# Kernel optimization log

Measured on AMD Instinct MI355X. Metric: run time of the kernel, lower is better.

## Reference

```python
import jax, jax.numpy as jnp
import numpy as np

B, N_OCR, N_OBJ, D, H, L, DFF = 64, 64, 192, 768, 12, 4, 2048
DH = D // H
EPS = 1e-5  # torch LayerNorm default


def _ln(x, g, b):
    m = jnp.mean(x, axis=-1, keepdims=True)
    v = jnp.mean(jnp.square(x - m), axis=-1, keepdims=True)
    return (x - m) * jax.lax.rsqrt(v + EPS) * g + b


def setup_inputs():
    key = jax.random.key(0)
    ks = iter(jax.random.split(key, 32))
    s = 0.02
    f = lambda shape: jax.random.normal(next(ks), shape, jnp.float32) * s
    return {
        "ocr_feats": jax.random.normal(next(ks), (B, N_OCR, D), jnp.float32),
        "obj_feats": jax.random.normal(next(ks), (B, N_OBJ, D), jnp.float32),
        "ocr_dvs": jax.random.uniform(next(ks), (B, N_OCR, 1), jnp.float32, 0.1, 2.0),
        "obj_dvs": jax.random.uniform(next(ks), (B, N_OBJ, 1), jnp.float32, 0.1, 2.0),
        # SemanticAttentionDeFUM projections
        "sa_wq": f((D, D)), "sa_bq": jnp.zeros((D,), jnp.float32),
        "sa_wk": f((D, D)), "sa_bk": jnp.zeros((D,), jnp.float32),
        "sa_wv": f((D, D)), "sa_bv": jnp.zeros((D,), jnp.float32),
        # outer LayerNorm
        "ln0_g": jnp.ones((D,), jnp.float32), "ln0_b": jnp.zeros((D,), jnp.float32),
        # stacked TransformerEncoder layer params (post-norm, batch_first)
        "qkv_w": f((L, 3 * D, D)), "qkv_b": jnp.zeros((L, 3 * D), jnp.float32),
        "out_w": f((L, D, D)), "out_b": jnp.zeros((L, D), jnp.float32),
        "ln1_g": jnp.ones((L, D), jnp.float32), "ln1_b": jnp.zeros((L, D), jnp.float32),
        "ff1_w": f((L, DFF, D)), "ff1_b": jnp.zeros((L, DFF), jnp.float32),
        "ff2_w": f((L, D, DFF)), "ff2_b": jnp.zeros((L, D), jnp.float32),
        "ln2_g": jnp.ones((L, D), jnp.float32), "ln2_b": jnp.zeros((L, D), jnp.float32),
    }


def reference(ocr_feats, obj_feats, ocr_dvs, obj_dvs,
              sa_wq, sa_bq, sa_wk, sa_bk, sa_wv, sa_bv,
              ln0_g, ln0_b,
              qkv_w, qkv_b, out_w, out_b, ln1_g, ln1_b,
              ff1_w, ff1_b, ff2_w, ff2_b, ln2_g, ln2_b):
    num_ocr = ocr_feats.shape[1]
    x = jnp.concatenate([ocr_feats, obj_feats], axis=1)       # B,N,D
    dv = jnp.concatenate([ocr_dvs, obj_dvs], axis=1)[..., 0]  # B,N
    # vectorized cal_relative_depth_map: log(max(dv_i,dv_j)/min(dv_i,dv_j))
    R = jnp.log(jnp.maximum(dv[:, :, None], dv[:, None, :]) /
                jnp.minimum(dv[:, :, None], dv[:, None, :]))  # B,N,N
    # semantic attention: scores A and values V
    q = jnp.einsum('bnd,ed->bne', x, sa_wq) + sa_bq
    k = jnp.einsum('bnd,ed->bne', x, sa_wk) + sa_bk
    v = jnp.einsum('bnd,ed->bne', x, sa_wv) + sa_bv
    A = jnp.einsum('bqd,bkd->bqk', q, k) / jnp.sqrt(jnp.float32(D))
    att = jax.nn.softmax(A + R, axis=-1)
    h = _ln(x + jnp.einsum('bqk,bkd->bqd', att, v), ln0_g, ln0_b)

    def layer(h, p):
        qw, qb, ow, ob, l1g, l1b, f1w, f1b, f2w, f2b, l2g, l2b = p
        Bn, N, _ = h.shape
        qkv = jnp.einsum('bnd,ed->bne', h, qw) + qb            # B,N,3D
        qh, kh, vh = jnp.split(qkv, 3, axis=-1)
        qh = qh.reshape(Bn, N, H, DH).transpose(0, 2, 1, 3)
        kh = kh.reshape(Bn, N, H, DH).transpose(0, 2, 1, 3)
        vh = vh.reshape(Bn, N, H, DH).transpose(0, 2, 1, 3)
        sc = jnp.einsum('bhqd,bhkd->bhqk', qh, kh) / jnp.sqrt(jnp.float32(DH))
        o = jnp.einsum('bhqk,bhkd->bhqd', jax.nn.softmax(sc, axis=-1), vh)
        o = o.transpose(0, 2, 1, 3).reshape(Bn, N, D)
        o = jnp.einsum('bnd,ed->bne', o, ow) + ob
        h = _ln(h + o, l1g, l1b)
        ff = jnp.einsum('bnd,fd->bnf', h, f1w) + f1b
        ff = jax.nn.gelu(ff, approximate=False)  # torch 'gelu' = exact erf gelu
        ff = jnp.einsum('bnf,df->bnd', ff, f2w) + f2b
        h = _ln(h + ff, l2g, l2b)
        return h, None

    h, _ = jax.lax.scan(layer, h, (qkv_w, qkv_b, out_w, out_b,
                                   ln1_g, ln1_b, ff1_w, ff1_b,
                                   ff2_w, ff2_b, ln2_g, ln2_b))
    return h[:, :num_ocr, :]
```

## Files before the change

kernel.cpp:

```cpp
#include <hip/hip_runtime.h>

typedef unsigned short u16;
typedef __bf16 bf16_t;
typedef bf16_t bf16x8 __attribute__((ext_vector_type(8)));
typedef float f32x4 __attribute__((ext_vector_type(4)));
typedef unsigned int u32x4 __attribute__((ext_vector_type(4)));
typedef u16 u16x4 __attribute__((ext_vector_type(4)));

#define GL_LDS16(gp, lp)                                              \
  __builtin_amdgcn_global_load_lds(                                   \
      (const __attribute__((address_space(1))) void*)(gp),            \
      (__attribute__((address_space(3))) void*)(lp), 16, 0, 0)

__device__ __forceinline__ u16 f2bf(float f) {
  unsigned u = __builtin_bit_cast(unsigned, f);
  u += 0x7fff + ((u >> 16) & 1);
  return (u16)(u >> 16);
}
__device__ __forceinline__ float bf2f(u16 h) {
  unsigned u = ((unsigned)h) << 16;
  return __builtin_bit_cast(float, u);
}
__device__ __forceinline__ float wredSum(float v) {
#pragma unroll
  for (int m = 32; m; m >>= 1) v += __shfl_xor(v, m);
  return v;
}

__global__ __launch_bounds__(256, 3) void gemmq(
    const u16* __restrict__ A, const u16* __restrict__ B,
    const float* __restrict__ bias, u16* __restrict__ C,
    int K, int N, int gx, int gy, int act, int tstore) {
  __shared__ __align__(16) char sm[3 * 16384];
  const int tid = threadIdx.x;
  const int l = tid & 63, w = tid >> 6, lg = l >> 4, li = l & 15;
  const int wr = w >> 1, wc = w & 1;
  const int TOT = gx * gy;
  int tix = blockIdx.x;
  if (tix >= TOT) return;
  const int G = gx >> 3;

  const long rowK64 = (long)64 * K;
  const long saoff = (long)(tid >> 2) * K + (((tid & 3) ^ ((tid >> 3) & 3)) << 3);
  const int t16 = tid * 16;

#define STAGE(bi_, Ap_, Bp_, kt_)                                      \
  do {                                                                 \
    char* lb_ = sm + (bi_) * 16384;                                    \
    const u16* ga_ = (Ap_) + saoff + ((long)(kt_) << 5);               \
    GL_LDS16(ga_, lb_ + t16);                                          \
    GL_LDS16(ga_ + rowK64, lb_ + 4096 + t16);                          \
    const u16* gb_ = (Bp_) + saoff + ((long)(kt_) << 5);               \
    GL_LDS16(gb_, lb_ + 8192 + t16);                                   \
    GL_LDS16(gb_ + rowK64, lb_ + 12288 + t16);                         \
  } while (0)

#define VM4 asm volatile("s_waitcnt vmcnt(4)" ::: "memory")
#define VM0 asm volatile("s_waitcnt vmcnt(0)" ::: "memory")

  int aof[4], bof[4];
#pragma unroll
  for (int f = 0; f < 4; ++f) {
    int ra = wr * 64 + f * 16 + li;
    aof[f] = ra * 64 + ((lg ^ ((ra >> 1) & 3)) << 4);
    int rb = wc * 64 + f * 16 + li;
    bof[f] = 8192 + rb * 64 + ((lg ^ ((rb >> 1) & 3)) << 4);
  }

  int mt, nt;
  const u16 *cA, *cB;
  { int xc = tix & 7, lo = tix >> 3;
    mt = xc * G + lo % G; nt = lo / G;
    cA = A + (long)mt * 128 * K; cB = B + (long)nt * 128 * K; }
  int nxt = tix + 768;
  int hasn = nxt < TOT;
  int nmt = 0, nnt = 0;
  const u16 *nA = cA, *nB = cB;
  if (hasn) { int xc = nxt & 7, lo = nxt >> 3;
    nmt = xc * G + lo % G; nnt = lo / G;
    nA = A + (long)nmt * 128 * K; nB = B + (long)nnt * 128 * K; }

  const int NT = K >> 5;
  f32x4 acc[4][4] = {};
  STAGE(0, cA, cB, 0); STAGE(1, cA, cB, 1);
  int bi = 0;

  for (;;) {
    for (int s = 0; s < NT; ++s) {
      int bi2 = bi + 2; if (bi2 >= 3) bi2 -= 3;
      const char* ab = sm + bi * 16384;
      if (s == NT - 1 && !hasn) VM0; else VM4;
      __builtin_amdgcn_s_barrier();
      asm volatile("" ::: "memory");
      int s2 = s + 2;
      if (s2 < NT) STAGE(bi2, cA, cB, s2);
      else if (hasn) STAGE(bi2, nA, nB, s2 - NT);
      bf16x8 af[4], bq[4];
#pragma unroll
      for (int f = 0; f < 4; ++f) {
        af[f] = __builtin_bit_cast(bf16x8, *(const u32x4*)(ab + aof[f]));
        bq[f] = __builtin_bit_cast(bf16x8, *(const u32x4*)(ab + bof[f]));
      }
      __builtin_amdgcn_s_setprio(1);
#pragma unroll
      for (int fi = 0; fi < 4; ++fi)
#pragma unroll
        for (int fj = 0; fj < 4; ++fj)
          acc[fi][fj] = __builtin_amdgcn_mfma_f32_16x16x32_bf16(af[fi], bq[fj], acc[fi][fj], 0, 0, 0);
      __builtin_amdgcn_s_setprio(0);
      bi = bi + 1; if (bi == 3) bi = 0;
    }
    {
      long row0 = (long)mt * 128 + wr * 64;
      int col0 = nt * 128 + wc * 64;
#pragma unroll
      for (int fi = 0; fi < 4; ++fi) {
#pragma unroll
        for (int fj = 0; fj < 4; ++fj) {
          int c = col0 + fj * 16 + li;
          float bv = bias ? bias[c] : 0.f;
#pragma unroll
          for (int r = 0; r < 4; ++r) {
            float v = acc[fi][fj][r] + bv;
            if (act) v = 0.5f * v * (1.f + erff(v * 0.70710678118f));
            long row = row0 + fi * 16 + lg * 4 + r;
            long idx = tstore ? ((row >> 8) * 196608 + (long)c * 256 + (row & 255))
                              : (row * (long)N + c);
            C[idx] = f2bf(v);
          }
          acc[fi][fj] = (f32x4){0.f, 0.f, 0.f, 0.f};
        }
      }
    }
    if (!hasn) break;
    VM0;
    mt = nmt; nt = nnt; cA = nA; cB = nB;
    tix = nxt; nxt += 768; hasn = nxt < TOT;
    if (hasn) { int xc = nxt & 7, lo = nxt >> 3;
      nmt = xc * G + lo % G; nnt = lo / G;
      nA = A + (long)nmt * 128 * K; nB = B + (long)nnt * 128 * K; }
  }
#undef STAGE
#undef VM4
#undef VM0
}

__global__ __launch_bounds__(256) void gemm_bt(
    const u16* __restrict__ A, const u16* __restrict__ B,
    const float* __restrict__ bias, const float* __restrict__ logdv,
    float* __restrict__ Cf, u16* __restrict__ Cb,
    int K, int ldc, long sA, long sB, long sC, float alpha, int act, int tstore) {
  __shared__ __align__(16) u16 As[2][128 * 32];
  __shared__ __align__(16) u16 Bs[2][128 * 32];
  int tid = threadIdx.x, w = tid >> 6, l = tid & 63, lg = l >> 4, li = l & 15;
  int wr = w >> 1, wc = w & 1;
  long bz = blockIdx.z;
  const u16* Ab = A + bz * sA + (long)blockIdx.x * 128 * K;
  const u16* Bb = B + bz * sB + (long)blockIdx.y * 128 * K;

  int sr = tid >> 2, ss = tid & 3;
  long ga0 = (long)sr * K + ((ss ^ ((sr >> 1) & 3)) << 3);
  long gstep = (long)K << 6;

  int aoff[4], boff[4];
#pragma unroll
  for (int i = 0; i < 4; ++i) {
    int ra = wr * 64 + i * 16 + li;
    aoff[i] = ra * 64 + ((lg ^ ((ra >> 1) & 3)) << 4);
    int rb = wc * 64 + i * 16 + li;
    boff[i] = rb * 64 + ((lg ^ ((rb >> 1) & 3)) << 4);
  }

  f32x4 acc[4][4] = {};
  int wb = w * 1024;

  GL_LDS16(Ab + ga0, (char*)As + wb);
  GL_LDS16(Ab + ga0 + gstep, (char*)As + 4096 + wb);
  GL_LDS16(Bb + ga0, (char*)Bs + wb);
  GL_LDS16(Bb + ga0 + gstep, (char*)Bs + 4096 + wb);
  __syncthreads();

  int T = K >> 5;
  int bsel = 0;
  for (int kt = 0; kt < T; ++kt) {
    if (kt + 1 < T) {
      long ko = (long)(kt + 1) << 5;
      char* an = (char*)As + (bsel ^ 1) * 8192;
      char* bn = (char*)Bs + (bsel ^ 1) * 8192;
      GL_LDS16(Ab + ga0 + ko, an + wb);
      GL_LDS16(Ab + ga0 + gstep + ko, an + 4096 + wb);
      GL_LDS16(Bb + ga0 + ko, bn + wb);
      GL_LDS16(Bb + ga0 + gstep + ko, bn + 4096 + wb);
    }
    char* ac = (char*)As + bsel * 8192;
    char* bc = (char*)Bs + bsel * 8192;
    bf16x8 af[4], bq[4];
#pragma unroll
    for (int i = 0; i < 4; ++i) {
      af[i] = __builtin_bit_cast(bf16x8, *(const u32x4*)(ac + aoff[i]));
      bq[i] = __builtin_bit_cast(bf16x8, *(const u32x4*)(bc + boff[i]));
    }
#pragma unroll
    for (int i = 0; i < 4; ++i)
#pragma unroll
      for (int j = 0; j < 4; ++j)
        acc[i][j] = __builtin_amdgcn_mfma_f32_16x16x32_bf16(af[i], bq[j], acc[i][j], 0, 0, 0);
    __syncthreads();
    bsel ^= 1;
  }

  long row0 = (long)blockIdx.x * 128 + wr * 64;
  int col0 = blockIdx.y * 128 + wc * 64;
  float* cf = Cf ? Cf + bz * sC : (float*)0;
  u16* cb = Cb ? Cb + bz * sC : (u16*)0;
  const float* ldv = logdv ? logdv + bz * 256 : (const float*)0;
#pragma unroll
  for (int i = 0; i < 4; ++i) {
    long rb0 = row0 + i * 16 + lg * 4;
#pragma unroll
    for (int j = 0; j < 4; ++j) {
      int c = col0 + j * 16 + li;
      float bv = bias ? bias[c] : 0.f;
      float lj = ldv ? ldv[c] : 0.f;
#pragma unroll
      for (int r = 0; r < 4; ++r) {
        float v = acc[i][j][r] * alpha + bv;
        if (ldv) v += fabsf(ldv[rb0 + r] - lj);
        if (act) v = 0.5f * v * (1.f + erff(v * 0.70710678118f));
        long row = rb0 + r;
        long idx = tstore ? ((row >> 8) * 196608 + (long)c * 256 + (row & 255))
                          : (row * ldc + c);
        if (cf) cf[idx] = v;
        if (cb) cb[idx] = f2bf(v);
      }
    }
  }
}

__global__ __launch_bounds__(256) void mha_k(const u16* __restrict__ qkv, u16* __restrict__ obf) {
  __shared__ __align__(16) u16 Ks[256 * 64];
  __shared__ __align__(16) u16 Vt[64 * 256];
  int b = blockIdx.y;
  int h = blockIdx.x >> 2, qt = blockIdx.x & 3;
  int tid = threadIdx.x, w = tid >> 6, l = tid & 63, lg = l >> 4, li = l & 15;
  const u16* kb_ = qkv + (long)b * 256 * 2304 + 768 + h * 64;
  const u16* vb_ = qkv + (long)b * 256 * 2304 + 1536 + h * 64;
#pragma unroll
  for (int it = 0; it < 8; ++it) {
    int c = it * 256 + tid; int n = c >> 3, sl = c & 7;
    u32x4 d = *(const u32x4*)(kb_ + (long)n * 2304 + sl * 8);
    *(u32x4*)((char*)Ks + n * 128 + ((sl ^ (n & 7)) << 4)) = d;
  }
#pragma unroll
  for (int it = 0; it < 8; ++it) {
    int c = it * 256 + tid; int n = c >> 3, sl = c & 7;
    u32x4 dv = *(const u32x4*)(vb_ + (long)n * 2304 + sl * 8);
    const u16* pe = (const u16*)&dv;
#pragma unroll
    for (int j = 0; j < 8; ++j) {
      int dd = sl * 8 + j;
      *(u16*)((char*)Vt + dd * 512 + (((n >> 3) ^ (dd & 7)) << 4) + (n & 7) * 2) = pe[j];
    }
  }
  __syncthreads();

  long qrow = (long)b * 256 + qt * 64 + w * 16 + li;
  const u16* qp = qkv + qrow * 2304 + h * 64;
  bf16x8 qf0 = __builtin_bit_cast(bf16x8, *(const u32x4*)(qp + lg * 8));
  bf16x8 qf1 = __builtin_bit_cast(bf16x8, *(const u32x4*)(qp + 32 + lg * 8));

  f32x4 sacc[16] = {};
#pragma unroll
  for (int jt = 0; jt < 16; ++jt) {
    int j = jt * 16 + li;
    u32x4 k0 = *(const u32x4*)((char*)Ks + j * 128 + ((lg ^ (j & 7)) << 4));
    u32x4 k1 = *(const u32x4*)((char*)Ks + j * 128 + (((4 + lg) ^ (j & 7)) << 4));
    sacc[jt] = __builtin_amdgcn_mfma_f32_16x16x32_bf16(qf0, __builtin_bit_cast(bf16x8, k0), sacc[jt], 0, 0, 0);
    sacc[jt] = __builtin_amdgcn_mfma_f32_16x16x32_bf16(qf1, __builtin_bit_cast(bf16x8, k1), sacc[jt], 0, 0, 0);
  }
#pragma unroll
  for (int jt = 0; jt < 16; ++jt) sacc[jt] = sacc[jt] * 0.125f;

  float rinv[4];
#pragma unroll
  for (int r = 0; r < 4; ++r) {
    float m = -1e30f;
#pragma unroll
    for (int jt = 0; jt < 16; ++jt) m = fmaxf(m, sacc[jt][r]);
#pragma unroll
    for (int mk = 1; mk < 16; mk <<= 1) m = fmaxf(m, __shfl_xor(m, mk));
    float s = 0.f;
#pragma unroll
    for (int jt = 0; jt < 16; ++jt) { float e = __expf(sacc[jt][r] - m); sacc[jt][r] = e; s += e; }
#pragma unroll
    for (int mk = 1; mk < 16; mk <<= 1) s += __shfl_xor(s, mk);
    rinv[r] = 1.f / s;
  }
  __syncthreads();
  char* Ps = (char*)Ks + w * 8192;
#pragma unroll
  for (int jt = 0; jt < 16; ++jt) {
    int j = jt * 16 + li;
#pragma unroll
    for (int r = 0; r < 4; ++r) {
      int i = lg * 4 + r;
      *(u16*)(Ps + i * 512 + (((j >> 3) ^ (i & 7)) << 4) + (j & 7) * 2) = f2bf(sacc[jt][r]);
    }
  }
  __syncthreads();
  f32x4 oacc[4] = {};
#pragma unroll
  for (int kb2 = 0; kb2 < 8; ++kb2) {
    int sl = kb2 * 4 + lg;
    u32x4 pa = *(const u32x4*)(Ps + li * 512 + ((sl ^ (li & 7)) << 4));
#pragma unroll
    for (int dt = 0; dt < 4; ++dt) {
      int dd = dt * 16 + li;
      u32x4 vv = *(const u32x4*)((char*)Vt + dd * 512 + ((sl ^ (dd & 7)) << 4));
      oacc[dt] = __builtin_amdgcn_mfma_f32_16x16x32_bf16(__builtin_bit_cast(bf16x8, pa),
                                                         __builtin_bit_cast(bf16x8, vv), oacc[dt], 0, 0, 0);
    }
  }
  long orow = (long)b * 256 + qt * 64 + w * 16;
#pragma unroll
  for (int dt = 0; dt < 4; ++dt)
#pragma unroll
    for (int r = 0; r < 4; ++r) {
      float vvv = oacc[dt][r] * rinv[r];
      obf[(orow + lg * 4 + r) * 768 + h * 64 + dt * 16 + li] = f2bf(vvv);
    }
}

__global__ __launch_bounds__(256) void ln_k(const u16* __restrict__ X, const u16* __restrict__ Rr,
                                            const float* __restrict__ g, const float* __restrict__ bb,
                                            u16* __restrict__ O) {
  long row = (long)blockIdx.x * 4 + (threadIdx.x >> 6);
  int l = threadIdx.x & 63;
  const u16* x = X + row * 768;
  const u16* rr = Rr + row * 768;
  f32x4 v[3];
  float s = 0.f;
#pragma unroll
  for (int i = 0; i < 3; ++i) {
    u16x4 xv = *(const u16x4*)(x + i * 256 + l * 4);
    u16x4 rv = *(const u16x4*)(rr + i * 256 + l * 4);
    f32x4 t;
#pragma unroll
    for (int j = 0; j < 4; ++j) t[j] = bf2f(xv[j]) + bf2f(rv[j]);
    v[i] = t;
    s += t[0] + t[1] + t[2] + t[3];
  }
  float mean = wredSum(s) * (1.f / 768.f);
  float q = 0.f;
#pragma unroll
  for (int i = 0; i < 3; ++i) {
#pragma unroll
    for (int j = 0; j < 4; ++j) { v[i][j] -= mean; q += v[i][j] * v[i][j]; }
  }
  float inv = rsqrtf(wredSum(q) * (1.f / 768.f) + 1e-5f);
#pragma unroll
  for (int i = 0; i < 3; ++i) {
    f32x4 gv = *(const f32x4*)(g + i * 256 + l * 4);
    f32x4 bv = *(const f32x4*)(bb + i * 256 + l * 4);
    u16x4 ob;
#pragma unroll
    for (int j = 0; j < 4; ++j) ob[j] = f2bf(v[i][j] * inv * gv[j] + bv[j]);
    *(u16x4*)(O + row * 768 + i * 256 + l * 4) = ob;
  }
}

__global__ __launch_bounds__(256) void smax_k(const float* __restrict__ S, u16* __restrict__ P) {
  long row = (long)blockIdx.x * 4 + (threadIdx.x >> 6);
  int l = threadIdx.x & 63;
  f32x4 v = *(const f32x4*)(S + row * 256 + l * 4);
  float m = fmaxf(fmaxf(v[0], v[1]), fmaxf(v[2], v[3]));
#pragma unroll
  for (int mk = 1; mk < 64; mk <<= 1) m = fmaxf(m, __shfl_xor(m, mk));
  float e0 = __expf(v[0] - m), e1 = __expf(v[1] - m), e2 = __expf(v[2] - m), e3 = __expf(v[3] - m);
  float s = wredSum(e0 + e1 + e2 + e3);
  float rn = 1.f / s;
  u16x4 o; o[0] = f2bf(e0 * rn); o[1] = f2bf(e1 * rn); o[2] = f2bf(e2 * rn); o[3] = f2bf(e3 * rn);
  *(u16x4*)(P + row * 256 + l * 4) = o;
}

__global__ __launch_bounds__(256) void conv_k(const float* __restrict__ in, u16* __restrict__ out, long n4) {
  long i = (long)blockIdx.x * 256 + threadIdx.x;
  if (i >= n4) return;
  f32x4 v = *(const f32x4*)(in + i * 4);
  u16x4 o; o[0] = f2bf(v[0]); o[1] = f2bf(v[1]); o[2] = f2bf(v[2]); o[3] = f2bf(v[3]);
  *(u16x4*)(out + i * 4) = o;
}

__global__ __launch_bounds__(256) void concat_k(const float* __restrict__ ocr, const float* __restrict__ obj,
                                                u16* __restrict__ xb) {
  long i = (long)blockIdx.x * 256 + threadIdx.x;
  if (i >= 16384L * 192) return;
  long row = i / 192; int c4 = (int)(i % 192);
  int b = (int)(row >> 8), n = (int)(row & 255);
  const float* src = (n < 64) ? (ocr + ((long)(b * 64 + n)) * 768) : (obj + ((long)(b * 192 + n - 64)) * 768);
  f32x4 v = *(const f32x4*)(src + c4 * 4);
  u16x4 o; o[0] = f2bf(v[0]); o[1] = f2bf(v[1]); o[2] = f2bf(v[2]); o[3] = f2bf(v[3]);
  *(u16x4*)(xb + row * 768 + c4 * 4) = o;
}

__global__ __launch_bounds__(256) void logdv_k(const float* __restrict__ ocr_dv, const float* __restrict__ obj_dv,
                                               float* __restrict__ out) {
  int i = blockIdx.x * 256 + threadIdx.x;
  if (i >= 16384) return;
  int b = i >> 8, n = i & 255;
  float dv = (n < 64) ? ocr_dv[b * 64 + n] : obj_dv[b * 192 + n - 64];
  out[i] = logf(dv);
}

__global__ __launch_bounds__(256) void slice_k(const u16* __restrict__ H, float* __restrict__ O) {
  long i = (long)blockIdx.x * 256 + threadIdx.x;
  if (i >= 786432) return;
  long idx = i * 4;
  long row = idx / 768; int c = (int)(idx % 768);
  long b = row >> 6, n = row & 63;
  u16x4 v = *(const u16x4*)(H + ((b * 256 + n) * 768 + c));
  f32x4 o; o[0] = bf2f(v[0]); o[1] = bf2f(v[1]); o[2] = bf2f(v[2]); o[3] = bf2f(v[3]);
  *(f32x4*)(O + idx) = o;
}

extern "C" void kernel_launch(void* const* d_in, const int* in_sizes, int n_in,
                              void* d_out, int out_size, void* d_ws, size_t ws_size,
                              hipStream_t stream) {
  const float* ocr = (const float*)d_in[0];
  const float* obj = (const float*)d_in[1];
  const float* ocr_dv = (const float*)d_in[2];
  const float* obj_dv = (const float*)d_in[3];
  const float* sa_wq = (const float*)d_in[4];
  const float* sa_bq = (const float*)d_in[5];
  const float* sa_wk = (const float*)d_in[6];
  const float* sa_bk = (const float*)d_in[7];
  const float* sa_wv = (const float*)d_in[8];
  const float* sa_bv = (const float*)d_in[9];
  const float* ln0_g = (const float*)d_in[10];
  const float* ln0_b = (const float*)d_in[11];
  const float* qkv_w = (const float*)d_in[12];
  const float* qkv_b = (const float*)d_in[13];
  const float* out_w = (const float*)d_in[14];
  const float* out_b = (const float*)d_in[15];
  const float* ln1_g = (const float*)d_in[16];
  const float* ln1_b = (const float*)d_in[17];
  const float* ff1_w = (const float*)d_in[18];
  const float* ff1_b = (const float*)d_in[19];
  const float* ff2_w = (const float*)d_in[20];
  const float* ff2_b = (const float*)d_in[21];
  const float* ln2_g = (const float*)d_in[22];
  const float* ln2_b = (const float*)d_in[23];

  char* ws = (char*)d_ws;
  u16* HB = (u16*)ws;
  float* LDV = (float*)(ws + 25165824);
  u16* WCV = (u16*)(ws + 25231360);
  char* SCR = ws + 36241408;

  const int bigws = ws_size >= (size_t)137953280;

  auto cv = [&](const float* src, long elems, u16* dst) {
    long n4 = elems >> 2;
    conv_k<<<dim3((unsigned)((n4 + 255) / 256)), dim3(256), 0, stream>>>(src, dst, n4);
  };

  concat_k<<<12288, 256, 0, stream>>>(ocr, obj, HB);
  logdv_k<<<64, 256, 0, stream>>>(ocr_dv, obj_dv, LDV);

  const float SSC = 0.03608439182435161f;

  cv(sa_wq, 589824, WCV);
  cv(sa_wk, 589824, WCV + 589824);
  cv(sa_wv, 589824, WCV + 1179648);

  if (bigws) {
    u16* Qf = (u16*)SCR;
    u16* Kf = (u16*)(SCR + 25165824);
    u16* VTf = (u16*)(SCR + 50331648);
    float* Sfc = (float*)(SCR + 75497472);
    u16* Pc = (u16*)(SCR + 83886080);
    u16* ATTc = (u16*)(SCR + 88080384);
    gemmq<<<768, 256, 0, stream>>>(HB, WCV, sa_bq, Qf, 768, 768, 128, 6, 0, 0);
    gemmq<<<768, 256, 0, stream>>>(HB, WCV + 589824, sa_bk, Kf, 768, 768, 128, 6, 0, 0);
    gemmq<<<768, 256, 0, stream>>>(HB, WCV + 1179648, sa_bv, VTf, 768, 768, 128, 6, 0, 1);
    for (int c = 0; c < 2; ++c) {
      long base = (long)c * 8192;
      gemm_bt<<<dim3(2, 2, 32), 256, 0, stream>>>(Qf + base * 768, Kf + base * 768, nullptr,
                                                  LDV + c * 8192, Sfc, nullptr, 768, 256,
                                                  196608, 196608, 65536, SSC, 0, 0);
      smax_k<<<2048, 256, 0, stream>>>(Sfc, Pc);
      gemm_bt<<<dim3(2, 6, 32), 256, 0, stream>>>(Pc, VTf + base * 768, nullptr, nullptr,
                                                  nullptr, ATTc, 256, 768, 65536, 196608, 196608, 1.f, 0, 0);
      ln_k<<<2048, 256, 0, stream>>>(HB + base * 768, ATTc, ln0_g, ln0_b, HB + base * 768);
    }
    u16* QKVf = (u16*)SCR;
    u16* Of = (u16*)(SCR + 75497472);
    u16* PRf = (u16*)SCR;
    u16* FFf = (u16*)(SCR + 25165824);
    for (int l = 0; l < 4; ++l) {
      cv(qkv_w + (long)l * 1769472, 1769472, WCV);
      cv(out_w + (long)l * 589824, 589824, WCV + 1769472);
      cv(ff1_w + (long)l * 1572864, 1572864, WCV + 2359296);
      cv(ff2_w + (long)l * 1572864, 1572864, WCV + 3932160);
      gemmq<<<768, 256, 0, stream>>>(HB, WCV, qkv_b + l * 2304, QKVf, 768, 2304, 128, 18, 0, 0);
      mha_k<<<dim3(48, 64), 256, 0, stream>>>(QKVf, Of);
      gemmq<<<768, 256, 0, stream>>>(Of, WCV + 1769472, out_b + l * 768, PRf, 768, 768, 128, 6, 0, 0);
      ln_k<<<4096, 256, 0, stream>>>(HB, PRf, ln1_g + l * 768, ln1_b + l * 768, HB);
      gemmq<<<768, 256, 0, stream>>>(HB, WCV + 2359296, ff1_b + l * 2048, FFf, 768, 2048, 128, 16, 1, 0);
      gemmq<<<768, 256, 0, stream>>>(FFf, WCV + 3932160, ff2_b + l * 768, PRf, 2048, 768, 128, 6, 0, 0);
      ln_k<<<4096, 256, 0, stream>>>(HB, PRf, ln2_g + l * 768, ln2_b + l * 768, HB);
    }
  } else {
    for (int c = 0; c < 2; ++c) {
      long base = (long)c * 8192;
      u16* Qc = (u16*)SCR;
      u16* Kc = (u16*)(SCR + 12582912);
      u16* VTc = (u16*)(SCR + 25165824);
      float* Sfc = (float*)(SCR + 37748736);
      u16* Pc = (u16*)(SCR + 46137344);
      u16* ATTc = (u16*)(SCR + 50331648);
      gemmq<<<768, 256, 0, stream>>>(HB + base * 768, WCV, sa_bq, Qc, 768, 768, 64, 6, 0, 0);
      gemmq<<<768, 256, 0, stream>>>(HB + base * 768, WCV + 589824, sa_bk, Kc, 768, 768, 64, 6, 0, 0);
      gemmq<<<768, 256, 0, stream>>>(HB + base * 768, WCV + 1179648, sa_bv, VTc, 768, 768, 64, 6, 0, 1);
      gemm_bt<<<dim3(2, 2, 32), 256, 0, stream>>>(Qc, Kc, nullptr, LDV + c * 8192,
                                                  Sfc, nullptr, 768, 256, 196608, 196608, 65536, SSC, 0, 0);
      smax_k<<<2048, 256, 0, stream>>>(Sfc, Pc);
      gemm_bt<<<dim3(2, 6, 32), 256, 0, stream>>>(Pc, VTc, nullptr, nullptr,
                                                  nullptr, ATTc, 256, 768, 65536, 196608, 196608, 1.f, 0, 0);
      ln_k<<<2048, 256, 0, stream>>>(HB + base * 768, ATTc, ln0_g, ln0_b, HB + base * 768);
    }
    for (int l = 0; l < 4; ++l) {
      cv(qkv_w + (long)l * 1769472, 1769472, WCV);
      cv(out_w + (long)l * 589824, 589824, WCV + 1769472);
      cv(ff1_w + (long)l * 1572864, 1572864, WCV + 2359296);
      cv(ff2_w + (long)l * 1572864, 1572864, WCV + 3932160);
      for (int c = 0; c < 2; ++c) {
        long base = (long)c * 8192;
        u16* QKVc = (u16*)SCR;
        u16* Oc = (u16*)(SCR + 37748736);
        u16* PRc = (u16*)(SCR + 50331648);
        u16* FFc = (u16*)SCR;
        gemmq<<<768, 256, 0, stream>>>(HB + base * 768, WCV, qkv_b + l * 2304, QKVc, 768, 2304, 64, 18, 0, 0);
        mha_k<<<dim3(48, 32), 256, 0, stream>>>(QKVc, Oc);
        gemmq<<<768, 256, 0, stream>>>(Oc, WCV + 1769472, out_b + l * 768, PRc, 768, 768, 64, 6, 0, 0);
        ln_k<<<2048, 256, 0, stream>>>(HB + base * 768, PRc, ln1_g + l * 768, ln1_b + l * 768, HB + base * 768);
        gemmq<<<768, 256, 0, stream>>>(HB + base * 768, WCV + 2359296, ff1_b + l * 2048, FFc, 768, 2048, 64, 16, 1, 0);
        gemmq<<<768, 256, 0, stream>>>(FFc, WCV + 3932160, ff2_b + l * 768, PRc, 2048, 768, 64, 6, 0, 0);
        ln_k<<<2048, 256, 0, stream>>>(HB + base * 768, PRc, ln2_g + l * 768, ln2_b + l * 768, HB + base * 768);
      }
    }
  }
  slice_k<<<3072, 256, 0, stream>>>(HB, (float*)d_out);
}
```

Baseline: 1.728 ms.

## Load A fragments directly from global into registers, stage only B in LDS

The persistent GEMM kernel no longer stages the A tile through LDS. Each wave loads its A MFMA fragments straight from global memory into registers, double-buffered across k-steps, while only B goes through the triple-buffered LDS ring. This halves LDS traffic and footprint and could raise occupancy. The cost is that each wave fetches A from global itself, with wait counts that now mix A register loads with B LDS loads, and A reads are uncoalesced 16-byte row strided accesses.

```diff
diff --git a/kernel.cpp b/kernel.cpp
--- a/kernel.cpp
+++ b/kernel.cpp
@@ -31,7 +31,7 @@
     const u16* __restrict__ A, const u16* __restrict__ B,
     const float* __restrict__ bias, u16* __restrict__ C,
     int K, int N, int gx, int gy, int act, int tstore) {
-  __shared__ __align__(16) char sm[3 * 16384];
+  __shared__ __align__(16) char sm[3 * 8192];
   const int tid = threadIdx.x;
   const int l = tid & 63, w = tid >> 6, lg = l >> 4, li = l & 15;
   const int wr = w >> 1, wc = w & 1;
@@ -44,28 +44,27 @@
   const long saoff = (long)(tid >> 2) * K + (((tid & 3) ^ ((tid >> 3) & 3)) << 3);
   const int t16 = tid * 16;
 
-#define STAGE(bi_, Ap_, Bp_, kt_)                                      \
+#define STAGEB(bi_, Bp_, kt_)                                          \
   do {                                                                 \
-    char* lb_ = sm + (bi_) * 16384;                                    \
-    const u16* ga_ = (Ap_) + saoff + ((long)(kt_) << 5);               \
-    GL_LDS16(ga_, lb_ + t16);                                          \
-    GL_LDS16(ga_ + rowK64, lb_ + 4096 + t16);                          \
+    char* lb_ = sm + (bi_) * 8192;                                     \
     const u16* gb_ = (Bp_) + saoff + ((long)(kt_) << 5);               \
-    GL_LDS16(gb_, lb_ + 8192 + t16);                                   \
-    GL_LDS16(gb_ + rowK64, lb_ + 12288 + t16);                         \
+    GL_LDS16(gb_, lb_ + t16);                                          \
+    GL_LDS16(gb_ + rowK64, lb_ + 4096 + t16);                          \
   } while (0)
 
-#define VM4 asm volatile("s_waitcnt vmcnt(4)" ::: "memory")
+#define VM2 asm volatile("s_waitcnt vmcnt(2)" ::: "memory")
 #define VM0 asm volatile("s_waitcnt vmcnt(0)" ::: "memory")
 
-  int aof[4], bof[4];
+  int bof[4];
 #pragma unroll
   for (int f = 0; f < 4; ++f) {
-    int ra = wr * 64 + f * 16 + li;
-    aof[f] = ra * 64 + ((lg ^ ((ra >> 1) & 3)) << 4);
     int rb = wc * 64 + f * 16 + li;
-    bof[f] = 8192 + rb * 64 + ((lg ^ ((rb >> 1) & 3)) << 4);
-  }
+    bof[f] = rb * 64 + ((lg ^ ((rb >> 1) & 3)) << 4);
+  }
+  long arow[4];
+#pragma unroll
+  for (int f = 0; f < 4; ++f)
+    arow[f] = (long)(wr * 64 + f * 16 + li) * K + lg * 8;
 
   int mt, nt;
   const u16 *cA, *cB;
@@ -82,33 +81,51 @@
 
   const int NT = K >> 5;
   f32x4 acc[4][4] = {};
-  STAGE(0, cA, cB, 0); STAGE(1, cA, cB, 1);
+  bf16x8 afA[4], afB[4];
+
+  STAGEB(0, cB, 0);
+#pragma unroll
+  for (int f = 0; f < 4; ++f)
+    afA[f] = __builtin_bit_cast(bf16x8, *(const u32x4*)(cA + arow[f]));
+  STAGEB(1, cB, 1);
   int bi = 0;
 
+#define ITER(s_, CUR, NXT)                                                     \
+  do {                                                                         \
+    int s_i = (s_);                                                            \
+    if (!hasn && s_i == NT - 1) VM0; else VM2;                                 \
+    int s1 = s_i + 1;                                                          \
+    if (s1 < NT) {                                                             \
+      _Pragma("unroll") for (int f = 0; f < 4; ++f)                            \
+        NXT[f] = __builtin_bit_cast(                                           \
+            bf16x8, *(const u32x4*)(cA + arow[f] + ((long)s1 << 5)));          \
+    } else if (hasn) {                                                         \
+      _Pragma("unroll") for (int f = 0; f < 4; ++f)                            \
+        NXT[f] = __builtin_bit_cast(                                           \
+            bf16x8, *(const u32x4*)(nA + arow[f] + ((long)(s1 - NT) << 5)));   \
+    }                                                                          \
+    __builtin_amdgcn_s_barrier();                                              \
+    asm volatile("" ::: "memory");                                             \
+    int s2 = s_i + 2, bi2 = bi + 2; if (bi2 >= 3) bi2 -= 3;                    \
+    if (s2 < NT) STAGEB(bi2, cB, s2);                                          \
+    else if (hasn) STAGEB(bi2, nB, s2 - NT);                                   \
+    const char* bb_ = sm + bi * 8192;                                          \
+    bf16x8 bq[4];                                                              \
+    _Pragma("unroll") for (int f = 0; f < 4; ++f)                              \
+      bq[f] = __builtin_bit_cast(bf16x8, *(const u32x4*)(bb_ + bof[f]));       \
+    __builtin_amdgcn_s_setprio(1);                                             \
+    _Pragma("unroll") for (int fi = 0; fi < 4; ++fi)                           \
+      _Pragma("unroll") for (int fj = 0; fj < 4; ++fj)                         \
+        acc[fi][fj] = __builtin_amdgcn_mfma_f32_16x16x32_bf16(                 \
+            CUR[fi], bq[fj], acc[fi][fj], 0, 0, 0);                            \
+    __builtin_amdgcn_s_setprio(0);                                             \
+    bi = bi + 1; if (bi == 3) bi = 0;                                          \
+  } while (0)
+
   for (;;) {
-    for (int s = 0; s < NT; ++s) {
-      int bi2 = bi + 2; if (bi2 >= 3) bi2 -= 3;
-      const char* ab = sm + bi * 16384;
-      if (s == NT - 1 && !hasn) VM0; else VM4;
-      __builtin_amdgcn_s_barrier();
-      asm volatile("" ::: "memory");
-      int s2 = s + 2;
-      if (s2 < NT) STAGE(bi2, cA, cB, s2);
-      else if (hasn) STAGE(bi2, nA, nB, s2 - NT);
-      bf16x8 af[4], bq[4];
-#pragma unroll
-      for (int f = 0; f < 4; ++f) {
-        af[f] = __builtin_bit_cast(bf16x8, *(const u32x4*)(ab + aof[f]));
-        bq[f] = __builtin_bit_cast(bf16x8, *(const u32x4*)(ab + bof[f]));
-      }
-      __builtin_amdgcn_s_setprio(1);
-#pragma unroll
-      for (int fi = 0; fi < 4; ++fi)
-#pragma unroll
-        for (int fj = 0; fj < 4; ++fj)
-          acc[fi][fj] = __builtin_amdgcn_mfma_f32_16x16x32_bf16(af[fi], bq[fj], acc[fi][fj], 0, 0, 0);
-      __builtin_amdgcn_s_setprio(0);
-      bi = bi + 1; if (bi == 3) bi = 0;
+    for (int s = 0; s < NT; s += 2) {
+      ITER(s, afA, afB);
+      ITER(s + 1, afB, afA);
     }
     {
       long row0 = (long)mt * 128 + wr * 64;
@@ -140,8 +157,9 @@
       nmt = xc * G + lo % G; nnt = lo / G;
       nA = A + (long)nmt * 128 * K; nB = B + (long)nnt * 128 * K; }
   }
-#undef STAGE
-#undef VM4
+#undef ITER
+#undef STAGEB
+#undef VM2
 #undef VM0
 }
 
```

After: 2.400 ms. +38.9%, slower.
